# Kernel optimization log

Hardware: AMD Instinct MI355X
Metric: run time of the kernel (lower is better)

The kernel has to match this reference:

```python
import jax, jax.numpy as jnp
from jax import lax
import numpy as np

H = 16        # hidden_size == input_size
L = 8         # num_layers


def _lstm_layer(x_seq, Wih, Whh, bih, bhh):
    # x_seq: [B, T, H] -> outputs [B, T, H]; PyTorch gate order i,f,g,o
    B = x_seq.shape[0]
    b = bih + bhh  # [4H]

    def step(carry, xt):
        h, c = carry
        gates = xt @ Wih.T + h @ Whh.T + b  # [B, 4H]
        i, f, g, o = jnp.split(gates, 4, axis=-1)
        c = jax.nn.sigmoid(f) * c + jax.nn.sigmoid(i) * jnp.tanh(g)
        h = jax.nn.sigmoid(o) * jnp.tanh(c)
        return (h, c), h

    h0 = jnp.zeros((B, H), x_seq.dtype)
    (_, _), hs = lax.scan(step, (h0, h0), jnp.swapaxes(x_seq, 0, 1))
    return jnp.swapaxes(hs, 0, 1)  # [B, T, H]


def setup_inputs() -> dict:
    key = jax.random.key(0)
    ks = jax.random.split(key, 9)
    s = 1.0 / np.sqrt(H)  # PyTorch default init scale
    x = jax.random.normal(ks[0], (2048, 512, H), dtype=jnp.float32)
    W_ih = jax.random.uniform(ks[1], (L, 4 * H, H), jnp.float32, -s, s)
    W_hh = jax.random.uniform(ks[2], (L, 4 * H, H), jnp.float32, -s, s)
    b_ih = jax.random.uniform(ks[3], (L, 4 * H), jnp.float32, -s, s)
    b_hh = jax.random.uniform(ks[4], (L, 4 * H), jnp.float32, -s, s)
    Wp = jax.random.uniform(ks[5], (3, H), jnp.float32, -s, s)
    bp = jax.random.uniform(ks[6], (3,), jnp.float32, -s, s)
    Wo = jax.random.uniform(ks[7], (3, H), jnp.float32, -s, s)
    bo = jax.random.uniform(ks[8], (3,), jnp.float32, -s, s)
    return {"x": x, "W_ih": W_ih, "W_hh": W_hh, "b_ih": b_ih, "b_hh": b_hh,
            "Wp": Wp, "bp": bp, "Wo": Wo, "bo": bo}


def reference(x, W_ih, W_hh, b_ih, b_hh, Wp, bp, Wo, bo):
    h = x
    for l in range(L):  # fixed small layer count
        h = _lstm_layer(h, W_ih[l], W_hh[l], b_ih[l], b_hh[l])
    last = h[:, -1, :]                       # [B, H]
    position = last @ Wp.T + bp              # [B, 3]
    orientation = jnp.tanh(last @ Wo.T + bo) # [B, 3]
    return jnp.concatenate((position, orientation), axis=1)  # [B, 6]
```

## Files before the change

### kernel.cpp

```cpp
#include <hip/hip_runtime.h>
#include <math.h>

typedef _Float16 f16x8 __attribute__((ext_vector_type(8)));
typedef float    f32x4 __attribute__((ext_vector_type(4)));

constexpr int kT    = 512;
constexpr int kH    = 16;
constexpr int kL    = 8;
constexpr int kG    = 64;
constexpr int kNB   = 8;
constexpr int kPad  = 24;
constexpr int kRows = 9;
constexpr int kSlots= 16;
constexpr int kLyr  = kL + 1;
constexpr int kSE   = kLyr * kRows * kPad;
constexpr int kIters= 33;

constexpr float kL2E = 1.4426950408889634f;

__device__ __forceinline__ float ex2(float w)  { return __builtin_amdgcn_exp2f(w); }
__device__ __forceinline__ float rcpf(float e) { return __builtin_amdgcn_rcpf(e); }

__global__ __launch_bounds__(1024, 4)
void lstm_w16(const float* __restrict__ x,
              const float* __restrict__ Wih, const float* __restrict__ Whh,
              const float* __restrict__ bih, const float* __restrict__ bhh,
              const float* __restrict__ Wp,  const float* __restrict__ bpos,
              const float* __restrict__ Wo,  const float* __restrict__ bori,
              float* __restrict__ out)
{
    const int tid  = threadIdx.x;
    const int wv   = tid >> 6;
    const int l    = wv >> 1;
    const int T    = wv & 1;
    const int lane = tid & 63;
    const int n    = lane & 15;
    const int q    = lane >> 4;
    const int bn   = n & 7;
    const bool bact = ((q >> 1) == (n >> 3));

    __shared__ __align__(16) _Float16 hb[kSlots][kLyr][kRows][kPad];

    {
        int* hz = (int*)&hb[0][0][0][0];
        for (int i = tid; i < (int)(sizeof(hb) / 4); i += 1024) hz[i] = 0;
    }
    __syncthreads();

    const float asc = ((n & 3) == 2) ? (-2.0f * kL2E) : (-kL2E);
    auto loadA = [&](const float* W) -> f16x8 {
        const int wrow = (n & 3) * 16 + (n >> 2) + 4 * (q >> 1) + 8 * T;
        const float* src = W + (size_t)l * kG * kH + wrow * kH;
        f16x8 a;
        #pragma unroll
        for (int j = 0; j < 8; ++j)
            a[j] = (_Float16)(asc * src[(q & 1) * 8 + j]);
        return a;
    };
    const f16x8 A1 = loadA(Wih);
    const f16x8 A2 = loadA(Whh);

    const int u0 = q + 4 * (n >> 3) + 8 * T;
    f32x4 bias;
    #pragma unroll
    for (int r = 0; r < 4; ++r) {
        const float sc = (r == 2) ? (-2.0f * kL2E) : (-kL2E);
        const int g0 = l * kG + r * 16 + u0;
        bias[r] = sc * (bih[g0] + bhh[g0]);
    }

    const int boff = (bact ? bn * kPad : 8 * kPad) + (q & 1) * 8;
    const _Float16* b1b = &hb[0][l    ][0][0] + boff;
    const _Float16* b2b = &hb[0][l + 1][0][0] + boff;
    _Float16* hw = &hb[0][l + 1][bn][u0];

    const int xu = (lane & 7) + 8 * T;
    _Float16* xw = &hb[0][0][lane >> 3][xu];
    const float* xg_ptr =
        x + ((size_t)(blockIdx.x * kNB + (lane >> 3)) * kT) * kH;
    float xa = 0.f, xb = 0.f, xc = 0.f;
    if (l == 0) {
        #pragma unroll
        for (int t = 0; t < 3; ++t)
            *(xw + ((t + 15) & 15) * kSE) = (_Float16)xg_ptr[t * kH + xu];
        xa = xg_ptr[3 * kH + xu];
        xb = xg_ptr[4 * kH + xu];
        xc = xg_ptr[5 * kH + xu];
    }
    __syncthreads();

    const f16x8 B1p = *(const f16x8*)(b1b + 15 * kSE);
    f32x4 dIn = __builtin_amdgcn_mfma_f32_16x16x32_f16(A1, B1p, bias, 0, 0, 0);

    float c0 = 0.f;
    const int tl = 2 * l;

    #pragma unroll 1
    for (int it = 0; it < kIters; ++it) {
        const int sb = it * 16;
        #pragma unroll
        for (int k = 0; k < 16; ++k) {
            const int s = sb + k;
            const int slotR = k * kSE;
            const int slotW = ((k + 1) & 15) * kSE;
            const int slotX = ((k + 2) & 15) * kSE;
            const bool active = ((unsigned)(s - tl) < (unsigned)kT);

            const f16x8 B2r = *(const f16x8*)(b2b + slotR);
            const f16x8 B1n = *(const f16x8*)(b1b + slotR);

            f32x4 d = __builtin_amdgcn_mfma_f32_16x16x32_f16(A2, B2r, dIn, 0, 0, 0);

            const float Ei = ex2(fminf(d[0], 40.0f));
            const float Ef = ex2(fminf(d[1], 40.0f));
            const float Eg = ex2(fminf(d[2], 40.0f));
            const float Eo = ex2(fminf(d[3], 60.0f));
            const float Dg = 1.0f + Eg;
            const float Df = 1.0f + Ef;
            const float P1  = fmaf(Ei, Dg, Dg);
            const float den = Df * P1;
            const float t2  = fmaf(-Eg, Df, Df);
            const float num = fmaf(c0, P1, t2);
            float cn = num * rcpf(den);
            cn = active ? cn : 0.0f;
            c0 = cn;
            const float ac = fminf(cn * (-2.0f * kL2E), 60.0f);
            const float Ec = ex2(ac);
            const float Do = 1.0f + Eo;
            const float R2 = rcpf(fmaf(Do, Ec, Do));
            const float h0 = fmaf(-Ec, R2, R2);

            *(hw + slotW) = (_Float16)h0;

            if (l == 0) {
                *(xw + slotX) = (_Float16)xa;
                xa = xb; xb = xc;
                int tn = s + 6; if (tn > kT - 1) tn = kT - 1;
                xc = xg_ptr[(size_t)tn * kH + xu];
            }

            dIn = __builtin_amdgcn_mfma_f32_16x16x32_f16(A1, B1n, bias, 0, 0, 0);

            asm volatile("s_waitcnt lgkmcnt(0)\n\ts_barrier" ::: "memory");
        }
    }

    __syncthreads();

    if (wv == 15) {
        const int bb = lane >> 3;
        const int r  = lane & 7;
        if (r < 6) {
            const bool  isP   = (r < 3);
            const float* wrow = isP ? (Wp + r * kH) : (Wo + (r - 3) * kH);
            float acc = isP ? bpos[r] : bori[r - 3];
            #pragma unroll
            for (int u = 0; u < kH; ++u)
                acc = fmaf((float)hb[14][kL][bb][u], wrow[u], acc);
            if (!isP) {
                const float Et = ex2(-2.0f * kL2E * acc);
                acc = fmaf(2.0f, rcpf(1.0f + Et), -1.0f);
            }
            out[(size_t)(blockIdx.x * kNB + bb) * 6 + r] = acc;
        }
    }
}

extern "C" void kernel_launch(void* const* d_in, const int* in_sizes, int n_in,
                              void* d_out, int out_size, void* d_ws, size_t ws_size,
                              hipStream_t stream) {
    const float* x    = (const float*)d_in[0];
    const float* Wih  = (const float*)d_in[1];
    const float* Whh  = (const float*)d_in[2];
    const float* bih  = (const float*)d_in[3];
    const float* bhh  = (const float*)d_in[4];
    const float* Wp   = (const float*)d_in[5];
    const float* bpos = (const float*)d_in[6];
    const float* Wo   = (const float*)d_in[7];
    const float* bori = (const float*)d_in[8];
    float* out = (float*)d_out;

    const int B = in_sizes[0] / (kT * kH);
    lstm_w16<<<dim3(B / kNB), dim3(1024), 0, stream>>>(x, Wih, Whh, bih, bhh,
                                                       Wp, bpos, Wo, bori, out);
}
```

Baseline: 282.5 us.

## Split waves by batch group instead of hidden half; prefetch recurrent operand across barrier

Each layer's two waves now each own 4 batch rows and all 16 hidden units, rather than 8 batch rows and half the hidden units. Each wave therefore issues two MFMAs per gate product (one per hidden half) and selects the relevant result per lane. The recurrent h operand is loaded right after this step's write and before the barrier, with the wait relaxed to lgkmcnt(1), to take LDS latency off the critical path. This doubles the MFMA work per wave and adds a select, and it depends on the barrier ordering being correct for the prefetched read.

```diff
diff --git a/kernel.cpp b/kernel.cpp
--- a/kernel.cpp
+++ b/kernel.cpp
@@ -20,24 +20,28 @@
 
 __device__ __forceinline__ float ex2(float w)  { return __builtin_amdgcn_exp2f(w); }
 __device__ __forceinline__ float rcpf(float e) { return __builtin_amdgcn_rcpf(e); }
+__device__ __forceinline__ void  cbar()        { asm volatile("" ::: "memory"); }
 
 __global__ __launch_bounds__(1024, 4)
-void lstm_w16(const float* __restrict__ x,
-              const float* __restrict__ Wih, const float* __restrict__ Whh,
-              const float* __restrict__ bih, const float* __restrict__ bhh,
-              const float* __restrict__ Wp,  const float* __restrict__ bpos,
-              const float* __restrict__ Wo,  const float* __restrict__ bori,
-              float* __restrict__ out)
+void lstm_bg(const float* __restrict__ x,
+             const float* __restrict__ Wih, const float* __restrict__ Whh,
+             const float* __restrict__ bih, const float* __restrict__ bhh,
+             const float* __restrict__ Wp,  const float* __restrict__ bpos,
+             const float* __restrict__ Wo,  const float* __restrict__ bori,
+             float* __restrict__ out)
 {
     const int tid  = threadIdx.x;
     const int wv   = tid >> 6;
-    const int l    = wv >> 1;
-    const int T    = wv & 1;
+    const int l    = wv & 7;
+    const int g    = wv >> 3;
     const int lane = tid & 63;
     const int n    = lane & 15;
     const int q    = lane >> 4;
-    const int bn   = n & 7;
-    const bool bact = ((q >> 1) == (n >> 3));
+    const int bl   = n & 3;
+    const int br   = 4 * g + bl;
+    const int g2   = (n >> 2) & 1;
+    const int hi   = n >> 3;
+    const bool bact = ((q >> 1) == g2);
 
     __shared__ __align__(16) _Float16 hb[kSlots][kLyr][kRows][kPad];
 
@@ -48,7 +52,7 @@
     __syncthreads();
 
     const float asc = ((n & 3) == 2) ? (-2.0f * kL2E) : (-kL2E);
-    auto loadA = [&](const float* W) -> f16x8 {
+    auto loadA = [&](const float* W, int T) -> f16x8 {
         const int wrow = (n & 3) * 16 + (n >> 2) + 4 * (q >> 1) + 8 * T;
         const float* src = W + (size_t)l * kG * kH + wrow * kH;
         f16x8 a;
@@ -57,40 +61,46 @@
             a[j] = (_Float16)(asc * src[(q & 1) * 8 + j]);
         return a;
     };
-    const f16x8 A1 = loadA(Wih);
-    const f16x8 A2 = loadA(Whh);
-
-    const int u0 = q + 4 * (n >> 3) + 8 * T;
-    f32x4 bias;
+    const f16x8 A1T0 = loadA(Wih, 0), A1T1 = loadA(Wih, 1);
+    const f16x8 A2T0 = loadA(Whh, 0), A2T1 = loadA(Whh, 1);
+
+    const int u0b = q + 4 * g2;
+    f32x4 biasT0, biasT1;
     #pragma unroll
     for (int r = 0; r < 4; ++r) {
         const float sc = (r == 2) ? (-2.0f * kL2E) : (-kL2E);
-        const int g0 = l * kG + r * 16 + u0;
-        bias[r] = sc * (bih[g0] + bhh[g0]);
-    }
-
-    const int boff = (bact ? bn * kPad : 8 * kPad) + (q & 1) * 8;
+        const int g0 = l * kG + r * 16 + u0b;
+        biasT0[r] = sc * (bih[g0] + bhh[g0]);
+        biasT1[r] = sc * (bih[g0 + 8] + bhh[g0 + 8]);
+    }
+
+    const int boff = (bact ? br * kPad : 8 * kPad) + (q & 1) * 8;
     const _Float16* b1b = &hb[0][l    ][0][0] + boff;
     const _Float16* b2b = &hb[0][l + 1][0][0] + boff;
-    _Float16* hw = &hb[0][l + 1][bn][u0];
-
-    const int xu = (lane & 7) + 8 * T;
-    _Float16* xw = &hb[0][0][lane >> 3][xu];
+    const int um = u0b + 8 * hi;
+    _Float16* hw = &hb[0][l + 1][br][um];
+    _Float16* xw = &hb[0][0][br][um];
+
     const float* xg_ptr =
-        x + ((size_t)(blockIdx.x * kNB + (lane >> 3)) * kT) * kH;
+        x + ((size_t)(blockIdx.x * kNB + br) * kT) * kH;
     float xa = 0.f, xb = 0.f, xc = 0.f;
     if (l == 0) {
         #pragma unroll
         for (int t = 0; t < 3; ++t)
-            *(xw + ((t + 15) & 15) * kSE) = (_Float16)xg_ptr[t * kH + xu];
-        xa = xg_ptr[3 * kH + xu];
-        xb = xg_ptr[4 * kH + xu];
-        xc = xg_ptr[5 * kH + xu];
+            *(xw + ((t + 15) & 15) * kSE) = (_Float16)xg_ptr[t * kH + um];
+        xa = xg_ptr[3 * kH + um];
+        xb = xg_ptr[4 * kH + um];
+        xc = xg_ptr[5 * kH + um];
     }
     __syncthreads();
 
     const f16x8 B1p = *(const f16x8*)(b1b + 15 * kSE);
-    f32x4 dIn = __builtin_amdgcn_mfma_f32_16x16x32_f16(A1, B1p, bias, 0, 0, 0);
+    f32x4 dInT0 = __builtin_amdgcn_mfma_f32_16x16x32_f16(A1T0, B1p, biasT0, 0, 0, 0);
+    f32x4 dInT1 = __builtin_amdgcn_mfma_f32_16x16x32_f16(A1T1, B1p, biasT1, 0, 0, 0);
+
+    f16x8 B2r;
+    #pragma unroll
+    for (int j = 0; j < 8; ++j) B2r[j] = (_Float16)0.f;
 
     float c0 = 0.f;
     const int tl = 2 * l;
@@ -106,10 +116,14 @@
             const int slotX = ((k + 2) & 15) * kSE;
             const bool active = ((unsigned)(s - tl) < (unsigned)kT);
 
-            const f16x8 B2r = *(const f16x8*)(b2b + slotR);
             const f16x8 B1n = *(const f16x8*)(b1b + slotR);
 
-            f32x4 d = __builtin_amdgcn_mfma_f32_16x16x32_f16(A2, B2r, dIn, 0, 0, 0);
+            f32x4 dT0 = __builtin_amdgcn_mfma_f32_16x16x32_f16(A2T0, B2r, dInT0, 0, 0, 0);
+            f32x4 dT1 = __builtin_amdgcn_mfma_f32_16x16x32_f16(A2T1, B2r, dInT1, 0, 0, 0);
+
+            f32x4 d;
+            #pragma unroll
+            for (int r = 0; r < 4; ++r) d[r] = hi ? dT1[r] : dT0[r];
 
             const float Ei = ex2(fminf(d[0], 40.0f));
             const float Ef = ex2(fminf(d[1], 40.0f));
@@ -136,12 +150,16 @@
                 *(xw + slotX) = (_Float16)xa;
                 xa = xb; xb = xc;
                 int tn = s + 6; if (tn > kT - 1) tn = kT - 1;
-                xc = xg_ptr[(size_t)tn * kH + xu];
+                xc = xg_ptr[(size_t)tn * kH + um];
             }
 
-            dIn = __builtin_amdgcn_mfma_f32_16x16x32_f16(A1, B1n, bias, 0, 0, 0);
-
-            asm volatile("s_waitcnt lgkmcnt(0)\n\ts_barrier" ::: "memory");
+            cbar();
+            B2r = *(const f16x8*)(b2b + slotW);
+
+            dInT0 = __builtin_amdgcn_mfma_f32_16x16x32_f16(A1T0, B1n, biasT0, 0, 0, 0);
+            dInT1 = __builtin_amdgcn_mfma_f32_16x16x32_f16(A1T1, B1n, biasT1, 0, 0, 0);
+
+            asm volatile("s_waitcnt lgkmcnt(1)\n\ts_barrier" ::: "memory");
         }
     }
 
@@ -181,6 +199,6 @@
     float* out = (float*)d_out;
 
     const int B = in_sizes[0] / (kT * kH);
-    lstm_w16<<<dim3(B / kNB), dim3(1024), 0, stream>>>(x, Wih, Whh, bih, bhh,
-                                                       Wp, bpos, Wo, bori, out);
+    lstm_bg<<<dim3(B / kNB), dim3(1024), 0, stream>>>(x, Wih, Whh, bih, bhh,
+                                                      Wp, bpos, Wo, bori, out);
 }
```

Result: slower. 305.1 us (+8.0%).

## Use one wave per layer with register-shuffled recurrent state and 16x16x16 MFMAs

Applied to the files above, without the earlier changes.

Each layer now runs on a single 64-lane wave instead of two, so a block has 512 threads. The recurrent h is passed within the wave through a shfl_xor, which keeps the Whh input off shared memory. The single 16x16x32 MFMA is replaced by four 16x16x16 MFMAs per operand, and each lane evaluates two gate-cell updates. The shared ring buffer shrinks to 8 slots. The aim is less LDS traffic and a smaller barrier scope per timestep, at the cost of more MFMA issues and twice the elementwise work per lane on the serial critical path.

```diff
diff --git a/kernel.cpp b/kernel.cpp
--- a/kernel.cpp
+++ b/kernel.cpp
@@ -1,28 +1,28 @@
 #include <hip/hip_runtime.h>
 #include <math.h>
 
-typedef _Float16 f16x8 __attribute__((ext_vector_type(8)));
+typedef _Float16 f16x4 __attribute__((ext_vector_type(4)));
+typedef _Float16 f16x2 __attribute__((ext_vector_type(2)));
 typedef float    f32x4 __attribute__((ext_vector_type(4)));
-
-constexpr int kT    = 512;
-constexpr int kH    = 16;
-constexpr int kL    = 8;
-constexpr int kG    = 64;
-constexpr int kNB   = 8;
-constexpr int kPad  = 24;
-constexpr int kRows = 9;
-constexpr int kSlots= 16;
-constexpr int kLyr  = kL + 1;
-constexpr int kSE   = kLyr * kRows * kPad;
-constexpr int kIters= 33;
+typedef float    f32x2 __attribute__((ext_vector_type(2)));
+
+constexpr int kT     = 512;
+constexpr int kH     = 16;
+constexpr int kL     = 8;
+constexpr int kNB    = 8;
+constexpr int kSlots = 8;
+constexpr int kLyr   = kL + 1;
+constexpr int kRow   = 16;
+constexpr int kSlotE = kLyr * kNB * kRow;
+constexpr int kIters = 33;
 
 constexpr float kL2E = 1.4426950408889634f;
 
 __device__ __forceinline__ float ex2(float w)  { return __builtin_amdgcn_exp2f(w); }
 __device__ __forceinline__ float rcpf(float e) { return __builtin_amdgcn_rcpf(e); }
 
-__global__ __launch_bounds__(1024, 4)
-void lstm_w16(const float* __restrict__ x,
+__global__ __launch_bounds__(512, 2)
+void lstm_rr8(const float* __restrict__ x,
               const float* __restrict__ Wih, const float* __restrict__ Whh,
               const float* __restrict__ bih, const float* __restrict__ bhh,
               const float* __restrict__ Wp,  const float* __restrict__ bpos,
@@ -30,116 +30,163 @@
               float* __restrict__ out)
 {
     const int tid  = threadIdx.x;
-    const int wv   = tid >> 6;
-    const int l    = wv >> 1;
-    const int T    = wv & 1;
+    const int l    = tid >> 6;
     const int lane = tid & 63;
     const int n    = lane & 15;
     const int q    = lane >> 4;
-    const int bn   = n & 7;
-    const bool bact = ((q >> 1) == (n >> 3));
-
-    __shared__ __align__(16) _Float16 hb[kSlots][kLyr][kRows][kPad];
+    const int b    = n & 7;
+    const int hi   = n >> 3;
+
+    __shared__ __align__(16) _Float16 hb[kSlots][kLyr][kNB][kRow];
 
     {
         int* hz = (int*)&hb[0][0][0][0];
-        for (int i = tid; i < (int)(sizeof(hb) / 4); i += 1024) hz[i] = 0;
+        for (int i = tid; i < (int)(sizeof(hb) / 4); i += 512) hz[i] = 0;
     }
     __syncthreads();
 
     const float asc = ((n & 3) == 2) ? (-2.0f * kL2E) : (-kL2E);
-    auto loadA = [&](const float* W) -> f16x8 {
-        const int wrow = (n & 3) * 16 + (n >> 2) + 4 * (q >> 1) + 8 * T;
-        const float* src = W + (size_t)l * kG * kH + wrow * kH;
-        f16x8 a;
-        #pragma unroll
-        for (int j = 0; j < 8; ++j)
-            a[j] = (_Float16)(asc * src[(q & 1) * 8 + j]);
-        return a;
-    };
-    const f16x8 A1 = loadA(Wih);
-    const f16x8 A2 = loadA(Whh);
-
-    const int u0 = q + 4 * (n >> 3) + 8 * T;
-    f32x4 bias;
+    f16x4 A1[4], A2[4];
+    f32x4 bias[4];
     #pragma unroll
-    for (int r = 0; r < 4; ++r) {
-        const float sc = (r == 2) ? (-2.0f * kL2E) : (-kL2E);
-        const int g0 = l * kG + r * 16 + u0;
-        bias[r] = sc * (bih[g0] + bhh[g0]);
-    }
-
-    const int boff = (bact ? bn * kPad : 8 * kPad) + (q & 1) * 8;
-    const _Float16* b1b = &hb[0][l    ][0][0] + boff;
-    const _Float16* b2b = &hb[0][l + 1][0][0] + boff;
-    _Float16* hw = &hb[0][l + 1][bn][u0];
-
-    const int xu = (lane & 7) + 8 * T;
-    _Float16* xw = &hb[0][0][lane >> 3][xu];
-    const float* xg_ptr =
-        x + ((size_t)(blockIdx.x * kNB + (lane >> 3)) * kT) * kH;
-    float xa = 0.f, xb = 0.f, xc = 0.f;
+    for (int p = 0; p < 4; ++p) {
+        const int wrow = (n & 3) * 16 + 4 * (n >> 2) + p;
+        const float* w1 = Wih + (size_t)l * 64 * kH + wrow * kH + 4 * q;
+        const float* w2 = Whh + (size_t)l * 64 * kH + wrow * kH + 4 * q;
+        #pragma unroll
+        for (int jj = 0; jj < 4; ++jj) {
+            A1[p][jj] = (_Float16)(asc * w1[jj]);
+            A2[p][jj] = (_Float16)(asc * w2[jj]);
+        }
+        #pragma unroll
+        for (int r = 0; r < 4; ++r) {
+            const float sc = (r == 2) ? (-2.0f * kL2E) : (-kL2E);
+            const int g0 = l * 64 + r * 16 + 4 * q + p;
+            bias[p][r] = sc * (bih[g0] + bhh[g0]);
+        }
+    }
+
+    const _Float16* b1base = &hb[0][l][b][4 * q];
+    _Float16* hwbase = &hb[0][l + 1][b][4 * q + 2 * hi];
+    _Float16* xwbase = &hb[0][0][b][4 * q + 2 * hi];
+
+    const float* xg = x + ((size_t)(blockIdx.x * kNB + b) * kT) * kH
+                        + 4 * q + 2 * hi;
+    f32x2 xr0 = {0.f, 0.f}, xr1 = {0.f, 0.f}, xr2 = {0.f, 0.f}, xr3 = {0.f, 0.f};
     if (l == 0) {
         #pragma unroll
-        for (int t = 0; t < 3; ++t)
-            *(xw + ((t + 15) & 15) * kSE) = (_Float16)xg_ptr[t * kH + xu];
-        xa = xg_ptr[3 * kH + xu];
-        xb = xg_ptr[4 * kH + xu];
-        xc = xg_ptr[5 * kH + xu];
+        for (int t = 0; t < 2; ++t) {
+            const f32x2 xv = *(const f32x2*)(xg + (size_t)t * kH);
+            f16x2 xh = { (_Float16)xv[0], (_Float16)xv[1] };
+            *(f16x2*)(&hb[6 + t][0][b][4 * q + 2 * hi]) = xh;
+        }
+        xr0 = *(const f32x2*)(xg + 2 * (size_t)kH);
+        xr1 = *(const f32x2*)(xg + 3 * (size_t)kH);
+        xr2 = *(const f32x2*)(xg + 4 * (size_t)kH);
+        xr3 = *(const f32x2*)(xg + 5 * (size_t)kH);
     }
     __syncthreads();
 
-    const f16x8 B1p = *(const f16x8*)(b1b + 15 * kSE);
-    f32x4 dIn = __builtin_amdgcn_mfma_f32_16x16x32_f16(A1, B1p, bias, 0, 0, 0);
-
-    float c0 = 0.f;
+    f32x4 dIn0, dIn1, dIn2, dIn3;
+    {
+        const f16x4 B1p = *(const f16x4*)(b1base + 6 * kSlotE);
+        dIn0 = __builtin_amdgcn_mfma_f32_16x16x16f16(A1[0], B1p, bias[0], 0, 0, 0);
+        dIn1 = __builtin_amdgcn_mfma_f32_16x16x16f16(A1[1], B1p, bias[1], 0, 0, 0);
+        dIn2 = __builtin_amdgcn_mfma_f32_16x16x16f16(A1[2], B1p, bias[2], 0, 0, 0);
+        dIn3 = __builtin_amdgcn_mfma_f32_16x16x16f16(A1[3], B1p, bias[3], 0, 0, 0);
+    }
+
+    f16x4 B2r = { (_Float16)0.f, (_Float16)0.f, (_Float16)0.f, (_Float16)0.f };
+    float cA = 0.f, cB = 0.f;
     const int tl = 2 * l;
 
     #pragma unroll 1
     for (int it = 0; it < kIters; ++it) {
-        const int sb = it * 16;
+        const int wb = it * 16;
         #pragma unroll
         for (int k = 0; k < 16; ++k) {
-            const int s = sb + k;
-            const int slotR = k * kSE;
-            const int slotW = ((k + 1) & 15) * kSE;
-            const int slotX = ((k + 2) & 15) * kSE;
-            const bool active = ((unsigned)(s - tl) < (unsigned)kT);
-
-            const f16x8 B2r = *(const f16x8*)(b2b + slotR);
-            const f16x8 B1n = *(const f16x8*)(b1b + slotR);
-
-            f32x4 d = __builtin_amdgcn_mfma_f32_16x16x32_f16(A2, B2r, dIn, 0, 0, 0);
-
-            const float Ei = ex2(fminf(d[0], 40.0f));
-            const float Ef = ex2(fminf(d[1], 40.0f));
-            const float Eg = ex2(fminf(d[2], 40.0f));
-            const float Eo = ex2(fminf(d[3], 60.0f));
-            const float Dg = 1.0f + Eg;
-            const float Df = 1.0f + Ef;
-            const float P1  = fmaf(Ei, Dg, Dg);
-            const float den = Df * P1;
-            const float t2  = fmaf(-Eg, Df, Df);
-            const float num = fmaf(c0, P1, t2);
-            float cn = num * rcpf(den);
-            cn = active ? cn : 0.0f;
-            c0 = cn;
-            const float ac = fminf(cn * (-2.0f * kL2E), 60.0f);
-            const float Ec = ex2(ac);
-            const float Do = 1.0f + Eo;
-            const float R2 = rcpf(fmaf(Do, Ec, Do));
-            const float h0 = fmaf(-Ec, R2, R2);
-
-            *(hw + slotW) = (_Float16)h0;
+            const int w = wb + k;
+            const bool active = ((unsigned)(w - tl) < (unsigned)kT);
+
+            const f16x4 B1n = *(const f16x4*)(b1base + ((k + 7) & 7) * kSlotE);
+
+            f32x4 d0 = __builtin_amdgcn_mfma_f32_16x16x16f16(A2[0], B2r, dIn0, 0, 0, 0);
+            f32x4 d1 = __builtin_amdgcn_mfma_f32_16x16x16f16(A2[1], B2r, dIn1, 0, 0, 0);
+            f32x4 d2 = __builtin_amdgcn_mfma_f32_16x16x16f16(A2[2], B2r, dIn2, 0, 0, 0);
+            f32x4 d3 = __builtin_amdgcn_mfma_f32_16x16x16f16(A2[3], B2r, dIn3, 0, 0, 0);
+
+            f32x4 dA, dB;
+            #pragma unroll
+            for (int r = 0; r < 4; ++r) {
+                dA[r] = hi ? d2[r] : d0[r];
+                dB[r] = hi ? d3[r] : d1[r];
+            }
+
+            float hAf, hBf;
+            {
+                const float Ei = ex2(fminf(dA[0], 40.0f));
+                const float Ef = ex2(fminf(dA[1], 40.0f));
+                const float Eg = ex2(fminf(dA[2], 40.0f));
+                const float Eo = ex2(fminf(dA[3], 60.0f));
+                const float Dg = 1.0f + Eg;
+                const float Df = 1.0f + Ef;
+                const float P1  = fmaf(Ei, Dg, Dg);
+                const float den = Df * P1;
+                const float t2  = fmaf(-Eg, Df, Df);
+                const float num = fmaf(cA, P1, t2);
+                float cn = num * rcpf(den);
+                cn = active ? cn : 0.0f;
+                cA = cn;
+                const float ac = fminf(cn * (-2.0f * kL2E), 60.0f);
+                const float Ec = ex2(ac);
+                const float Do = 1.0f + Eo;
+                const float R2 = rcpf(fmaf(Do, Ec, Do));
+                hAf = fmaf(-Ec, R2, R2);
+            }
+            {
+                const float Ei = ex2(fminf(dB[0], 40.0f));
+                const float Ef = ex2(fminf(dB[1], 40.0f));
+                const float Eg = ex2(fminf(dB[2], 40.0f));
+                const float Eo = ex2(fminf(dB[3], 60.0f));
+                const float Dg = 1.0f + Eg;
+                const float Df = 1.0f + Ef;
+                const float P1  = fmaf(Ei, Dg, Dg);
+                const float den = Df * P1;
+                const float t2  = fmaf(-Eg, Df, Df);
+                const float num = fmaf(cB, P1, t2);
+                float cn = num * rcpf(den);
+                cn = active ? cn : 0.0f;
+                cB = cn;
+                const float ac = fminf(cn * (-2.0f * kL2E), 60.0f);
+                const float Ec = ex2(ac);
+                const float Do = 1.0f + Eo;
+                const float R2 = rcpf(fmaf(Do, Ec, Do));
+                hBf = fmaf(-Ec, R2, R2);
+            }
+
+            f16x2 hp = { (_Float16)hAf, (_Float16)hBf };
+            union { f16x2 h; int i; } uh; uh.h = hp;
+            const int own   = uh.i;
+            const int other = __shfl_xor(own, 8, 64);
+            union { int i[2]; f16x4 v; } ub;
+            ub.i[0] = hi ? other : own;
+            ub.i[1] = hi ? own : other;
+            B2r = ub.v;
+
+            *(f16x2*)(hwbase + (k & 7) * kSlotE) = hp;
 
             if (l == 0) {
-                *(xw + slotX) = (_Float16)xa;
-                xa = xb; xb = xc;
-                int tn = s + 6; if (tn > kT - 1) tn = kT - 1;
-                xc = xg_ptr[(size_t)tn * kH + xu];
-            }
-
-            dIn = __builtin_amdgcn_mfma_f32_16x16x32_f16(A1, B1n, bias, 0, 0, 0);
+                f16x2 xh = { (_Float16)xr0[0], (_Float16)xr0[1] };
+                *(f16x2*)(xwbase + (k & 7) * kSlotE) = xh;
+                xr0 = xr1; xr1 = xr2; xr2 = xr3;
+                int tn = w + 6; if (tn > kT - 1) tn = kT - 1;
+                xr3 = *(const f32x2*)(xg + (size_t)tn * kH);
+            }
+
+            dIn0 = __builtin_amdgcn_mfma_f32_16x16x16f16(A1[0], B1n, bias[0], 0, 0, 0);
+            dIn1 = __builtin_amdgcn_mfma_f32_16x16x16f16(A1[1], B1n, bias[1], 0, 0, 0);
+            dIn2 = __builtin_amdgcn_mfma_f32_16x16x16f16(A1[2], B1n, bias[2], 0, 0, 0);
+            dIn3 = __builtin_amdgcn_mfma_f32_16x16x16f16(A1[3], B1n, bias[3], 0, 0, 0);
 
             asm volatile("s_waitcnt lgkmcnt(0)\n\ts_barrier" ::: "memory");
         }
@@ -147,21 +194,23 @@
 
     __syncthreads();
 
-    if (wv == 15) {
-        const int bb = lane >> 3;
-        const int r  = lane & 7;
-        if (r < 6) {
-            const bool  isP   = (r < 3);
-            const float* wrow = isP ? (Wp + r * kH) : (Wo + (r - 3) * kH);
-            float acc = isP ? bpos[r] : bori[r - 3];
+    if (l == kL - 1 && lane < kNB) {
+        const int bb = lane;
+        float hreg[kH];
+        #pragma unroll
+        for (int u = 0; u < kH; ++u) hreg[u] = (float)hb[5][kL][bb][u];
+        #pragma unroll
+        for (int r = 0; r < 3; ++r) {
+            float accP = bpos[r], accO = bori[r];
             #pragma unroll
-            for (int u = 0; u < kH; ++u)
-                acc = fmaf((float)hb[14][kL][bb][u], wrow[u], acc);
-            if (!isP) {
-                const float Et = ex2(-2.0f * kL2E * acc);
-                acc = fmaf(2.0f, rcpf(1.0f + Et), -1.0f);
-            }
-            out[(size_t)(blockIdx.x * kNB + bb) * 6 + r] = acc;
+            for (int u = 0; u < kH; ++u) {
+                accP = fmaf(hreg[u], Wp[r * kH + u], accP);
+                accO = fmaf(hreg[u], Wo[r * kH + u], accO);
+            }
+            const float Et = ex2(-2.0f * kL2E * accO);
+            accO = fmaf(2.0f, rcpf(1.0f + Et), -1.0f);
+            out[(size_t)(blockIdx.x * kNB + bb) * 6 + r]     = accP;
+            out[(size_t)(blockIdx.x * kNB + bb) * 6 + 3 + r] = accO;
         }
     }
 }
@@ -181,6 +230,6 @@
     float* out = (float*)d_out;
 
     const int B = in_sizes[0] / (kT * kH);
-    lstm_w16<<<dim3(B / kNB), dim3(1024), 0, stream>>>(x, Wih, Whh, bih, bhh,
-                                                       Wp, bpos, Wo, bori, out);
+    lstm_rr8<<<dim3(B / kNB), dim3(512), 0, stream>>>(x, Wih, Whh, bih, bhh,
+                                                      Wp, bpos, Wo, bori, out);
 }
```

Measured after the change: 312.2 us. +10.5%, slower.
